# Performance work log

Hardware: AMD Instinct MI355X
Metric: run time of the kernel (lower is better)

Reference implementation:

```python
import jax, jax.numpy as jnp
import numpy as np

EPS = 1e-12  # torch F.normalize default eps
NUM_HEADS = 8


def _l2norm(t):
    # normalize along last (spatial) axis, matching F.normalize(dim=-1)
    n = jnp.linalg.norm(t, axis=-1, keepdims=True)
    return t / jnp.maximum(n, EPS)


def setup_inputs() -> dict:
    key = jax.random.key(0)
    ks = jax.random.split(key, 5)
    b, dim, qc, h, w = 16, 384, 192, 64, 64
    x = jax.random.normal(ks[0], (b, dim, h, w), dtype=jnp.float32)
    query = jax.random.normal(ks[1], (b, qc, h, w), dtype=jnp.float32)
    w_kv = jax.random.normal(ks[2], (2 * dim, dim), dtype=jnp.float32) * 0.05
    w_q = jax.random.normal(ks[3], (dim, qc), dtype=jnp.float32) * 0.05
    w_proj = jax.random.normal(ks[4], (dim, dim), dtype=jnp.float32) * 0.05
    temperature = jnp.ones((NUM_HEADS, 1, 1), dtype=jnp.float32)
    return {"x": x, "query": query, "w_kv": w_kv, "w_q": w_q,
            "w_proj": w_proj, "temperature": temperature}


def reference(x, query, w_kv, w_q, w_proj, temperature):
    b, c, h, w = x.shape
    hd = NUM_HEADS
    dc = c // hd  # per-head channel dim
    # 1x1 convs == channel GEMMs
    kv = jnp.einsum('oc,bchw->bohw', w_kv, x)          # [b, 2c, h, w]
    k, v = jnp.split(kv, 2, axis=1)                     # each [b, c, h, w]
    q = jnp.einsum('oc,bchw->bohw', w_q, query)         # [b, c, h, w]
    # split heads, flatten spatial: b (head c) h w -> b head c (h w)
    def heads(t):
        return t.reshape(b, hd, dc, h * w)
    q, k, v = heads(q), heads(k), heads(v)
    q = _l2norm(q)
    k = _l2norm(k)
    # channel-wise attention: [b, head, dc, dc]
    attn = jnp.einsum('bhcn,bhdn->bhcd', q, k) * temperature
    attn = jax.nn.softmax(attn, axis=-1)
    out = jnp.einsum('bhcd,bhdn->bhcn', attn, v)        # [b, head, dc, hw]
    out = out.reshape(b, c, h, w)
    out = jnp.einsum('oc,bchw->bohw', w_proj, out)
    return out
```

## Files before the change

kernel.cpp:

```cpp
#include <hip/hip_runtime.h>
#include <hip/hip_bf16.h>

typedef float f4 __attribute__((ext_vector_type(4)));
typedef short s8 __attribute__((ext_vector_type(8)));
typedef short s4 __attribute__((ext_vector_type(4)));

__device__ __forceinline__ short f2bf(float f) {
  union { float f; unsigned u; } v; v.f = f;
  unsigned r = v.u + 0x7fffu + ((v.u >> 16) & 1u);
  return (short)(r >> 16);
}
__device__ __forceinline__ void gl16(const short* g, short* l) {
  __builtin_amdgcn_global_load_lds(
      (const __attribute__((address_space(1))) unsigned*)g,
      (__attribute__((address_space(3))) unsigned*)l, 16, 0, 0);
}

template<int NKT, bool SUMSQ, bool OUTF32, bool SWZ>
__global__ __launch_bounds__(256)
void gemm4(const short* __restrict__ A_, long Asb, int lda,
           const short* __restrict__ B_, long Bsb, int ldb,
           void* __restrict__ O_, long Osb, int ldo,
           float* __restrict__ ss, int nbm, int nbn) {
  __shared__ __align__(16) short As[2][8192];
  __shared__ __align__(16) short Bs[2][8192];
  int f = blockIdx.x;
  if (SWZ) { const int cpx = gridDim.x >> 3; f = (f & 7) * cpx + (f >> 3); }
  const int m0 = (f % nbm) * 128;
  const int t2 = f / nbm;
  const int n0 = (t2 % nbn) * 128;
  const int bz = t2 / nbn;
  const short* Ag = A_ + (long)bz * Asb;
  const short* Bg = B_ + (long)bz * Bsb;

  const int tid = threadIdx.x, lane = tid & 63, wid = tid >> 6;
  const int l15 = lane & 15, lhi = lane >> 4;
  const int wm = (wid >> 1) * 64, wn = (wid & 1) * 64;
  const int srow = tid >> 3;
  const int skc = ((tid & 7) ^ (srow & 7)) * 8;

  f4 acc[4][4];
#pragma unroll
  for (int i = 0; i < 4; ++i)
#pragma unroll
    for (int j = 0; j < 4; ++j) acc[i][j] = (f4){0.f, 0.f, 0.f, 0.f};

#pragma unroll
  for (int it = 0; it < 4; ++it) {
    const int r = it * 32 + srow;
    gl16(Ag + (long)(m0 + r) * lda + skc, &As[0][(it * 256 + tid) * 8]);
    gl16(Bg + (long)(n0 + r) * ldb + skc, &Bs[0][(it * 256 + tid) * 8]);
  }
  if (NKT > 1) {
#pragma unroll
    for (int it = 0; it < 4; ++it) {
      const int r = it * 32 + srow;
      gl16(Ag + (long)(m0 + r) * lda + 64 + skc, &As[1][(it * 256 + tid) * 8]);
      gl16(Bg + (long)(n0 + r) * ldb + 64 + skc, &Bs[1][(it * 256 + tid) * 8]);
    }
  }

#pragma unroll
  for (int kt = 0; kt < NKT; ++kt) {
    const int cur = kt & 1;
    if (kt + 1 < NKT) asm volatile("s_waitcnt vmcnt(8)" ::: "memory");
    else              asm volatile("s_waitcnt vmcnt(0)" ::: "memory");
    __builtin_amdgcn_s_barrier();
    __builtin_amdgcn_sched_barrier(0);
#pragma unroll
    for (int kk = 0; kk < 2; ++kk) {
      const int cb = ((lhi + kk * 4) ^ (l15 & 7)) * 8;
      s8 af[4], bf[4];
#pragma unroll
      for (int i = 0; i < 4; ++i) {
        af[i] = *(const s8*)(&As[cur][(wm + i * 16 + l15) * 64 + cb]);
        bf[i] = *(const s8*)(&Bs[cur][(wn + i * 16 + l15) * 64 + cb]);
      }
#pragma unroll
      for (int mi = 0; mi < 4; ++mi)
#pragma unroll
        for (int ni = 0; ni < 4; ++ni)
          acc[mi][ni] = __builtin_amdgcn_mfma_f32_16x16x32_bf16(
              af[mi], bf[ni], acc[mi][ni], 0, 0, 0);
    }
    asm volatile("s_waitcnt lgkmcnt(0)" ::: "memory");
    __builtin_amdgcn_s_barrier();
    if (kt + 2 < NKT) {
      const int k2 = (kt + 2) * 64;
#pragma unroll
      for (int it = 0; it < 4; ++it) {
        const int r = it * 32 + srow;
        gl16(Ag + (long)(m0 + r) * lda + k2 + skc,
             &As[cur][(it * 256 + tid) * 8]);
        gl16(Bg + (long)(n0 + r) * ldb + k2 + skc,
             &Bs[cur][(it * 256 + tid) * 8]);
      }
    }
  }

#pragma unroll
  for (int mi = 0; mi < 4; ++mi)
#pragma unroll
    for (int r = 0; r < 4; ++r) {
      const int grow = m0 + wm + mi * 16 + lhi * 4 + r;
      if (SUMSQ) {
        float t = 0.f;
#pragma unroll
        for (int ni = 0; ni < 4; ++ni) { float v = acc[mi][ni][r]; t += v * v; }
        t += __shfl_xor(t, 1);
        t += __shfl_xor(t, 2);
        t += __shfl_xor(t, 4);
        t += __shfl_xor(t, 8);
        if (l15 == 0) atomicAdd(&ss[bz * 384 + grow], t);
      }
#pragma unroll
      for (int ni = 0; ni < 4; ++ni) {
        const int col = n0 + wn + ni * 16 + l15;
        const float v = acc[mi][ni][r];
        if (OUTF32)
          ((float*)O_)[(long)bz * Osb + (long)grow * ldo + col] = v;
        else
          ((short*)O_)[(long)bz * Osb + (long)grow * ldo + col] = f2bf(v);
      }
    }
}

__global__ __launch_bounds__(256)
void trans_k(const float* __restrict__ src, short* __restrict__ dst, int C) {
  __shared__ float Ls[64][65];
  const int tid = threadIdx.x;
  const int c0 = blockIdx.x * 64, s0 = blockIdx.y * 64;
  const long bb = (long)blockIdx.z * C * 4096;
  const int rr = tid >> 4;
  const int cq = (tid & 15) * 4;
#pragma unroll
  for (int it = 0; it < 4; ++it) {
    const int r = it * 16 + rr;
    f4 v = *(const f4*)(src + bb + (long)(c0 + r) * 4096 + s0 + cq);
    Ls[r][cq + 0] = v.x; Ls[r][cq + 1] = v.y;
    Ls[r][cq + 2] = v.z; Ls[r][cq + 3] = v.w;
  }
  __syncthreads();
  const long ob = (long)blockIdx.z * 4096 * C;
#pragma unroll
  for (int it = 0; it < 4; ++it) {
    const int sr = it * 16 + rr;
    s4 o;
#pragma unroll
    for (int j = 0; j < 4; ++j) o[j] = f2bf(Ls[cq + j][sr]);
    *(s4*)(&dst[ob + (long)(s0 + sr) * C + c0 + cq]) = o;
  }
}

__global__ __launch_bounds__(256)
void attn_k(const short* __restrict__ Kb, const short* __restrict__ Qb,
            float* __restrict__ Spart) {
  const int b = blockIdx.x, h = blockIdx.y, z = blockIdx.z;
  const int tid = threadIdx.x;
  const int lane = tid & 63, wid = tid >> 6;
  const int l15 = lane & 15, lhi = lane >> 4;
  const long base = ((long)b * 384 + h * 48) * 4096;

  f4 acc[3][3];
#pragma unroll
  for (int i = 0; i < 3; ++i)
#pragma unroll
    for (int j = 0; j < 3; ++j) acc[i][j] = (f4){0.f, 0.f, 0.f, 0.f};

  const int sb = z * 1024 + wid * 256;
  for (int st = 0; st < 8; ++st) {
    const int s0 = sb + st * 32 + lhi * 8;
    s8 qa[3], ka[3];
#pragma unroll
    for (int i = 0; i < 3; ++i) {
      qa[i] = *(const s8*)(Qb + base + (long)(i * 16 + l15) * 4096 + s0);
      ka[i] = *(const s8*)(Kb + base + (long)(i * 16 + l15) * 4096 + s0);
    }
#pragma unroll
    for (int mi = 0; mi < 3; ++mi)
#pragma unroll
      for (int ni = 0; ni < 3; ++ni)
        acc[mi][ni] = __builtin_amdgcn_mfma_f32_16x16x32_bf16(
            qa[mi], ka[ni], acc[mi][ni], 0, 0, 0);
  }
  __shared__ float Sl[2304];
  for (int i = tid; i < 2304; i += 256) Sl[i] = 0.f;
  __syncthreads();
#pragma unroll
  for (int mi = 0; mi < 3; ++mi)
#pragma unroll
    for (int ni = 0; ni < 3; ++ni)
#pragma unroll
      for (int r = 0; r < 4; ++r) {
        int c = mi * 16 + lhi * 4 + r;
        int d = ni * 16 + l15;
        atomicAdd(&Sl[c * 48 + d], acc[mi][ni][r]);
      }
  __syncthreads();
  float* op = Spart + (((long)z * 16 + b) * 8 + h) * 2304;
  for (int i = tid; i < 2304; i += 256) op[i] = Sl[i];
}

__global__ __launch_bounds__(256)
void softmax_k(const float* __restrict__ Spart, const float* __restrict__ ssq,
               const float* __restrict__ ssk, const float* __restrict__ temp,
               short* __restrict__ PT) {
  const int b = blockIdx.x, h = blockIdx.y, tid = threadIdx.x;
  __shared__ float L[2304];
  __shared__ float rq[48], rk[48], mrow[48], irow[48];
  if (tid < 48) {
    rq[tid] = 1.f / fmaxf(sqrtf(ssq[b * 384 + h * 48 + tid]), 1e-12f);
    rk[tid] = 1.f / fmaxf(sqrtf(ssk[b * 384 + h * 48 + tid]), 1e-12f);
  }
  __syncthreads();
  const float tp = temp[h];
  for (int i = tid; i < 2304; i += 256) {
    float v = 0.f;
#pragma unroll
    for (int z = 0; z < 4; ++z)
      v += Spart[(((long)z * 16 + b) * 8 + h) * 2304 + i];
    const int c = i / 48, d = i % 48;
    L[i] = v * rq[c] * rk[d] * tp;
  }
  __syncthreads();
  if (tid < 48) {
    float m = -1e30f;
    for (int d = 0; d < 48; ++d) m = fmaxf(m, L[tid * 48 + d]);
    float s = 0.f;
    for (int d = 0; d < 48; ++d) s += __expf(L[tid * 48 + d] - m);
    mrow[tid] = m;
    irow[tid] = 1.f / s;
  }
  __syncthreads();
  for (int i = tid; i < 18432; i += 256) {
    const int d = i / 384, c = i % 384;
    const int ch = c - h * 48;
    float p = 0.f;
    if (ch >= 0 && ch < 48) p = __expf(L[ch * 48 + d] - mrow[ch]) * irow[ch];
    PT[((long)b * 384 + h * 48 + d) * 384 + c] = f2bf(p);
  }
}

__global__ void wprep_k(const float* __restrict__ wkv, const float* __restrict__ wq,
                        const float* __restrict__ wp, short* __restrict__ wkb,
                        short* __restrict__ wvT, short* __restrict__ wqb,
                        short* __restrict__ wpb, float* __restrict__ ssqk) {
  const int i = blockIdx.x * 256 + threadIdx.x;
  if (i < 12288) ssqk[i] = 0.f;
  if (i < 147456) {
    wkb[i] = f2bf(wkv[i]);
  } else if (i < 294912) {
    const int t = i - 147456;
    wvT[t] = f2bf(wkv[(384 + (t % 384)) * 384 + t / 384]);
  } else if (i < 368640) {
    wqb[i - 294912] = f2bf(wq[i - 294912]);
  } else {
    wpb[i - 368640] = f2bf(wp[i - 368640]);
  }
}

extern "C" void kernel_launch(void* const* d_in, const int* in_sizes, int n_in,
                              void* d_out, int out_size, void* d_ws, size_t ws_size,
                              hipStream_t stream) {
  const float* x = (const float*)d_in[0];
  const float* query = (const float*)d_in[1];
  const float* w_kv = (const float*)d_in[2];
  const float* w_q = (const float*)d_in[3];
  const float* w_proj = (const float*)d_in[4];
  const float* temp = (const float*)d_in[5];

  char* w = (char*)d_ws;
  short* xT   = (short*)(w + 0);
  short* qT   = (short*)(w + 50331648);
  short* Kb   = (short*)(w + 75497472);
  short* Qb   = (short*)(w + 125829120);
  float* Spart= (float*)(w + 176160768);
  short* PTb  = (short*)(w + 195035136);
  short* Yb   = (short*)(w + 199753728);
  short* Nbb  = (short*)(w + 204472320);
  float* ssq  = (float*)(w + 209190912);
  float* ssk  = (float*)(w + 209215488);
  short* wkb  = (short*)(w + 209240064);
  short* wvT  = (short*)(w + 209534976);
  short* wqb  = (short*)(w + 209829888);
  short* wpb  = (short*)(w + 209977344);
  float* out  = (float*)d_out;

  wprep_k<<<2016, 256, 0, stream>>>(w_kv, w_q, w_proj, wkb, wvT, wqb, wpb, ssq);
  trans_k<<<dim3(6, 64, 16), 256, 0, stream>>>(x, xT, 384);
  trans_k<<<dim3(3, 64, 16), 256, 0, stream>>>(query, qT, 192);
  gemm4<3, true, false, true><<<1536, 256, 0, stream>>>(
      wqb, 0, 192, qT, 786432, 192, Qb, 1572864, 4096, ssq, 3, 32);
  gemm4<6, true, false, true><<<1536, 256, 0, stream>>>(
      wkb, 0, 384, xT, 1572864, 384, Kb, 1572864, 4096, ssk, 3, 32);
  attn_k<<<dim3(16, 8, 4), 256, 0, stream>>>(Kb, Qb, Spart);
  softmax_k<<<dim3(16, 8), 256, 0, stream>>>(Spart, ssq, ssk, temp, PTb);
  gemm4<6, false, false, false><<<144, 256, 0, stream>>>(
      wpb, 0, 384, PTb, 147456, 384, Yb, 147456, 384, nullptr, 3, 3);
  gemm4<6, false, false, false><<<144, 256, 0, stream>>>(
      Yb, 147456, 384, wvT, 0, 384, Nbb, 147456, 384, nullptr, 3, 3);
  gemm4<6, false, true, true><<<1536, 256, 0, stream>>>(
      Nbb, 147456, 384, xT, 1572864, 384, out, 1572864, 4096, nullptr, 3, 32);
}
```

Before: 229.8 us.

## Fuse Q/K projections with channel-attention scores into one kernel

```diff
diff --git a/kernel.cpp b/kernel.cpp
--- a/kernel.cpp
+++ b/kernel.cpp
@@ -16,12 +16,171 @@
       (__attribute__((address_space(3))) unsigned*)l, 16, 0, 0);
 }
 
-template<int NKT, bool SUMSQ, bool OUTF32, bool SWZ>
+__global__ __launch_bounds__(256)
+void kqa_k(const short* __restrict__ xT, const short* __restrict__ qT,
+           const short* __restrict__ wkb, const short* __restrict__ wqb,
+           float* __restrict__ Spart, float* __restrict__ ssq,
+           float* __restrict__ ssk) {
+  __shared__ __align__(16) short Bq[64 * 192];
+  __shared__ __align__(16) short Bx[64 * 384];
+  __shared__ __align__(16) short Qt[192 * 64];
+  __shared__ __align__(16) short Kt[192 * 64];
+  const int f = blockIdx.x;
+  const int sl = f & 63, hg = (f >> 6) & 1, b = f >> 7;
+  const int s0 = sl * 64;
+  const int tid = threadIdx.x, lane = tid & 63, w = tid >> 6;
+  const int l15 = lane & 15, lhi = lane >> 4;
+  const short* qTb = qT + ((long)b * 4096 + s0) * 192;
+  const short* xTb = xT + ((long)b * 4096 + s0) * 384;
+
+#pragma unroll
+  for (int i = 0; i < 6; ++i) {
+    const int q = i * 256 + tid, row = q / 24, c = q % 24;
+    gl16(qTb + row * 192 + ((c ^ (row & 7)) * 8), &Bq[q * 8]);
+  }
+#pragma unroll
+  for (int i = 0; i < 12; ++i) {
+    const int q = i * 256 + tid, row = q / 48, c = q % 48;
+    gl16(xTb + row * 384 + ((c ^ (row & 7)) * 8), &Bx[q * 8]);
+  }
+  asm volatile("s_waitcnt vmcnt(12)" ::: "memory");
+  __builtin_amdgcn_s_barrier();
+  __builtin_amdgcn_sched_barrier(0);
+
+  {
+    f4 acc[3][4];
+#pragma unroll
+    for (int i = 0; i < 3; ++i)
+#pragma unroll
+      for (int j = 0; j < 4; ++j) acc[i][j] = (f4){0.f, 0.f, 0.f, 0.f};
+#pragma unroll 2
+    for (int kk = 0; kk < 192; kk += 32) {
+      s8 af[3], bf[4];
+#pragma unroll
+      for (int mi = 0; mi < 3; ++mi)
+        af[mi] = *(const s8*)(wqb +
+            (long)(hg * 192 + w * 48 + mi * 16 + l15) * 192 + kk + lhi * 8);
+#pragma unroll
+      for (int ni = 0; ni < 4; ++ni) {
+        const int s_ = ni * 16 + l15;
+        bf[ni] = *(const s8*)(&Bq[s_ * 192 + ((((kk >> 3) + lhi) ^ (s_ & 7)) << 3)]);
+      }
+#pragma unroll
+      for (int mi = 0; mi < 3; ++mi)
+#pragma unroll
+        for (int ni = 0; ni < 4; ++ni)
+          acc[mi][ni] = __builtin_amdgcn_mfma_f32_16x16x32_bf16(
+              af[mi], bf[ni], acc[mi][ni], 0, 0, 0);
+    }
+#pragma unroll
+    for (int mi = 0; mi < 3; ++mi)
+#pragma unroll
+      for (int r = 0; r < 4; ++r) {
+        const int row = w * 48 + mi * 16 + lhi * 4 + r;
+        float t = 0.f;
+#pragma unroll
+        for (int ni = 0; ni < 4; ++ni) {
+          const int col = ni * 16 + l15;
+          const float v = acc[mi][ni][r];
+          Qt[row * 64 + (((col >> 3) ^ (row & 7)) << 3) + (col & 7)] = f2bf(v);
+          t += v * v;
+        }
+        t += __shfl_xor(t, 1); t += __shfl_xor(t, 2);
+        t += __shfl_xor(t, 4); t += __shfl_xor(t, 8);
+        if (l15 == 0) atomicAdd(&ssq[b * 384 + hg * 192 + row], t);
+      }
+  }
+
+  asm volatile("s_waitcnt vmcnt(0)" ::: "memory");
+  __builtin_amdgcn_s_barrier();
+  __builtin_amdgcn_sched_barrier(0);
+
+  {
+    f4 acc[3][4];
+#pragma unroll
+    for (int i = 0; i < 3; ++i)
+#pragma unroll
+      for (int j = 0; j < 4; ++j) acc[i][j] = (f4){0.f, 0.f, 0.f, 0.f};
+#pragma unroll 2
+    for (int kk = 0; kk < 384; kk += 32) {
+      s8 af[3], bf[4];
+#pragma unroll
+      for (int mi = 0; mi < 3; ++mi)
+        af[mi] = *(const s8*)(wkb +
+            (long)(hg * 192 + w * 48 + mi * 16 + l15) * 384 + kk + lhi * 8);
+#pragma unroll
+      for (int ni = 0; ni < 4; ++ni) {
+        const int s_ = ni * 16 + l15;
+        bf[ni] = *(const s8*)(&Bx[s_ * 384 + ((((kk >> 3) + lhi) ^ (s_ & 7)) << 3)]);
+      }
+#pragma unroll
+      for (int mi = 0; mi < 3; ++mi)
+#pragma unroll
+        for (int ni = 0; ni < 4; ++ni)
+          acc[mi][ni] = __builtin_amdgcn_mfma_f32_16x16x32_bf16(
+              af[mi], bf[ni], acc[mi][ni], 0, 0, 0);
+    }
+#pragma unroll
+    for (int mi = 0; mi < 3; ++mi)
+#pragma unroll
+      for (int r = 0; r < 4; ++r) {
+        const int row = w * 48 + mi * 16 + lhi * 4 + r;
+        float t = 0.f;
+#pragma unroll
+        for (int ni = 0; ni < 4; ++ni) {
+          const int col = ni * 16 + l15;
+          const float v = acc[mi][ni][r];
+          Kt[row * 64 + (((col >> 3) ^ (row & 7)) << 3) + (col & 7)] = f2bf(v);
+          t += v * v;
+        }
+        t += __shfl_xor(t, 1); t += __shfl_xor(t, 2);
+        t += __shfl_xor(t, 4); t += __shfl_xor(t, 8);
+        if (l15 == 0) atomicAdd(&ssk[b * 384 + hg * 192 + row], t);
+      }
+  }
+
+  {
+    f4 acc[3][3];
+#pragma unroll
+    for (int i = 0; i < 3; ++i)
+#pragma unroll
+      for (int j = 0; j < 3; ++j) acc[i][j] = (f4){0.f, 0.f, 0.f, 0.f};
+    const int hl = w * 48;
+#pragma unroll
+    for (int kk = 0; kk < 64; kk += 32) {
+      s8 qa[3], ka[3];
+#pragma unroll
+      for (int i = 0; i < 3; ++i) {
+        const int rr = hl + i * 16 + l15;
+        const int cb = (((kk >> 3) + lhi) ^ (rr & 7)) << 3;
+        qa[i] = *(const s8*)(&Qt[rr * 64 + cb]);
+        ka[i] = *(const s8*)(&Kt[rr * 64 + cb]);
+      }
+#pragma unroll
+      for (int mi = 0; mi < 3; ++mi)
+#pragma unroll
+        for (int ni = 0; ni < 3; ++ni)
+          acc[mi][ni] = __builtin_amdgcn_mfma_f32_16x16x32_bf16(
+              qa[mi], ka[ni], acc[mi][ni], 0, 0, 0);
+    }
+    float* Sp = Spart + (((long)(sl & 7) * 16 + b) * 8 + (hg * 4 + w)) * 2304;
+#pragma unroll
+    for (int mi = 0; mi < 3; ++mi)
+#pragma unroll
+      for (int ni = 0; ni < 3; ++ni)
+#pragma unroll
+        for (int r = 0; r < 4; ++r)
+          atomicAdd(&Sp[(mi * 16 + lhi * 4 + r) * 48 + ni * 16 + l15],
+                    acc[mi][ni][r]);
+  }
+}
+
+template<int NKT, bool OUTF32, bool SWZ>
 __global__ __launch_bounds__(256)
 void gemm4(const short* __restrict__ A_, long Asb, int lda,
            const short* __restrict__ B_, long Bsb, int ldb,
            void* __restrict__ O_, long Osb, int ldo,
-           float* __restrict__ ss, int nbm, int nbn) {
+           int nbm, int nbn) {
   __shared__ __align__(16) short As[2][8192];
   __shared__ __align__(16) short Bs[2][8192];
   int f = blockIdx.x;
@@ -103,16 +262,6 @@
 #pragma unroll
     for (int r = 0; r < 4; ++r) {
       const int grow = m0 + wm + mi * 16 + lhi * 4 + r;
-      if (SUMSQ) {
-        float t = 0.f;
-#pragma unroll
-        for (int ni = 0; ni < 4; ++ni) { float v = acc[mi][ni][r]; t += v * v; }
-        t += __shfl_xor(t, 1);
-        t += __shfl_xor(t, 2);
-        t += __shfl_xor(t, 4);
-        t += __shfl_xor(t, 8);
-        if (l15 == 0) atomicAdd(&ss[bz * 384 + grow], t);
-      }
 #pragma unroll
       for (int ni = 0; ni < 4; ++ni) {
         const int col = n0 + wn + ni * 16 + l15;
@@ -150,55 +299,6 @@
     for (int j = 0; j < 4; ++j) o[j] = f2bf(Ls[cq + j][sr]);
     *(s4*)(&dst[ob + (long)(s0 + sr) * C + c0 + cq]) = o;
   }
-}
-
-__global__ __launch_bounds__(256)
-void attn_k(const short* __restrict__ Kb, const short* __restrict__ Qb,
-            float* __restrict__ Spart) {
-  const int b = blockIdx.x, h = blockIdx.y, z = blockIdx.z;
-  const int tid = threadIdx.x;
-  const int lane = tid & 63, wid = tid >> 6;
-  const int l15 = lane & 15, lhi = lane >> 4;
-  const long base = ((long)b * 384 + h * 48) * 4096;
-
-  f4 acc[3][3];
-#pragma unroll
-  for (int i = 0; i < 3; ++i)
-#pragma unroll
-    for (int j = 0; j < 3; ++j) acc[i][j] = (f4){0.f, 0.f, 0.f, 0.f};
-
-  const int sb = z * 1024 + wid * 256;
-  for (int st = 0; st < 8; ++st) {
-    const int s0 = sb + st * 32 + lhi * 8;
-    s8 qa[3], ka[3];
-#pragma unroll
-    for (int i = 0; i < 3; ++i) {
-      qa[i] = *(const s8*)(Qb + base + (long)(i * 16 + l15) * 4096 + s0);
-      ka[i] = *(const s8*)(Kb + base + (long)(i * 16 + l15) * 4096 + s0);
-    }
-#pragma unroll
-    for (int mi = 0; mi < 3; ++mi)
-#pragma unroll
-      for (int ni = 0; ni < 3; ++ni)
-        acc[mi][ni] = __builtin_amdgcn_mfma_f32_16x16x32_bf16(
-            qa[mi], ka[ni], acc[mi][ni], 0, 0, 0);
-  }
-  __shared__ float Sl[2304];
-  for (int i = tid; i < 2304; i += 256) Sl[i] = 0.f;
-  __syncthreads();
-#pragma unroll
-  for (int mi = 0; mi < 3; ++mi)
-#pragma unroll
-    for (int ni = 0; ni < 3; ++ni)
-#pragma unroll
-      for (int r = 0; r < 4; ++r) {
-        int c = mi * 16 + lhi * 4 + r;
-        int d = ni * 16 + l15;
-        atomicAdd(&Sl[c * 48 + d], acc[mi][ni][r]);
-      }
-  __syncthreads();
-  float* op = Spart + (((long)z * 16 + b) * 8 + h) * 2304;
-  for (int i = tid; i < 2304; i += 256) op[i] = Sl[i];
 }
 
 __global__ __launch_bounds__(256)
@@ -217,7 +317,7 @@
   for (int i = tid; i < 2304; i += 256) {
     float v = 0.f;
 #pragma unroll
-    for (int z = 0; z < 4; ++z)
+    for (int z = 0; z < 8; ++z)
       v += Spart[(((long)z * 16 + b) * 8 + h) * 2304 + i];
     const int c = i / 48, d = i % 48;
     L[i] = v * rq[c] * rk[d] * tp;
@@ -244,9 +344,11 @@
 __global__ void wprep_k(const float* __restrict__ wkv, const float* __restrict__ wq,
                         const float* __restrict__ wp, short* __restrict__ wkb,
                         short* __restrict__ wvT, short* __restrict__ wqb,
-                        short* __restrict__ wpb, float* __restrict__ ssqk) {
+                        short* __restrict__ wpb, float* __restrict__ ssqk,
+                        float* __restrict__ Spart) {
   const int i = blockIdx.x * 256 + threadIdx.x;
   if (i < 12288) ssqk[i] = 0.f;
+  for (int j = i; j < 2359296; j += 516096) Spart[j] = 0.f;
   if (i < 147456) {
     wkb[i] = f2bf(wkv[i]);
   } else if (i < 294912) {
@@ -272,33 +374,28 @@
   char* w = (char*)d_ws;
   short* xT   = (short*)(w + 0);
   short* qT   = (short*)(w + 50331648);
-  short* Kb   = (short*)(w + 75497472);
-  short* Qb   = (short*)(w + 125829120);
-  float* Spart= (float*)(w + 176160768);
-  short* PTb  = (short*)(w + 195035136);
-  short* Yb   = (short*)(w + 199753728);
-  short* Nbb  = (short*)(w + 204472320);
-  float* ssq  = (float*)(w + 209190912);
-  float* ssk  = (float*)(w + 209215488);
-  short* wkb  = (short*)(w + 209240064);
-  short* wvT  = (short*)(w + 209534976);
-  short* wqb  = (short*)(w + 209829888);
-  short* wpb  = (short*)(w + 209977344);
+  float* Spart= (float*)(w + 75497472);
+  short* PTb  = (short*)(w + 84934656);
+  short* Yb   = (short*)(w + 89653248);
+  short* Nbb  = (short*)(w + 94371840);
+  float* ssq  = (float*)(w + 99090432);
+  float* ssk  = (float*)(w + 99115008);
+  short* wkb  = (short*)(w + 99139584);
+  short* wvT  = (short*)(w + 99434496);
+  short* wqb  = (short*)(w + 99729408);
+  short* wpb  = (short*)(w + 99876864);
   float* out  = (float*)d_out;
 
-  wprep_k<<<2016, 256, 0, stream>>>(w_kv, w_q, w_proj, wkb, wvT, wqb, wpb, ssq);
+  wprep_k<<<2016, 256, 0, stream>>>(w_kv, w_q, w_proj, wkb, wvT, wqb, wpb,
+                                    ssq, Spart);
   trans_k<<<dim3(6, 64, 16), 256, 0, stream>>>(x, xT, 384);
   trans_k<<<dim3(3, 64, 16), 256, 0, stream>>>(query, qT, 192);
-  gemm4<3, true, false, true><<<1536, 256, 0, stream>>>(
-      wqb, 0, 192, qT, 786432, 192, Qb, 1572864, 4096, ssq, 3, 32);
-  gemm4<6, true, false, true><<<1536, 256, 0, stream>>>(
-      wkb, 0, 384, xT, 1572864, 384, Kb, 1572864, 4096, ssk, 3, 32);
-  attn_k<<<dim3(16, 8, 4), 256, 0, stream>>>(Kb, Qb, Spart);
+  kqa_k<<<2048, 256, 0, stream>>>(xT, qT, wkb, wqb, Spart, ssq, ssk);
   softmax_k<<<dim3(16, 8), 256, 0, stream>>>(Spart, ssq, ssk, temp, PTb);
-  gemm4<6, false, false, false><<<144, 256, 0, stream>>>(
-      wpb, 0, 384, PTb, 147456, 384, Yb, 147456, 384, nullptr, 3, 3);
-  gemm4<6, false, false, false><<<144, 256, 0, stream>>>(
-      Yb, 147456, 384, wvT, 0, 384, Nbb, 147456, 384, nullptr, 3, 3);
-  gemm4<6, false, true, true><<<1536, 256, 0, stream>>>(
-      Nbb, 147456, 384, xT, 1572864, 384, out, 1572864, 4096, nullptr, 3, 32);
-}
+  gemm4<6, false, false><<<144, 256, 0, stream>>>(
+      wpb, 0, 384, PTb, 147456, 384, Yb, 147456, 384, 3, 3);
+  gemm4<6, false, false><<<144, 256, 0, stream>>>(
+      Yb, 147456, 384, wvT, 0, 384, Nbb, 147456, 384, 3, 3);
+  gemm4<6, true, true><<<1536, 256, 0, stream>>>(
+      Nbb, 147456, 384, xT, 1572864, 384, out, 1572864, 4096, 3, 32);
+}
```

Measured after the change: 282.8 us. 1.23x slower.

## Merge transpose and K/Q GEMM launches, fuse softmax with w_proj GEMM

Applied to the files above, without the earlier changes.

```diff
diff --git a/kernel.cpp b/kernel.cpp
--- a/kernel.cpp
+++ b/kernel.cpp
@@ -16,12 +16,114 @@
       (__attribute__((address_space(3))) unsigned*)l, 16, 0, 0);
 }
 
-template<int NKT, bool SUMSQ, bool OUTF32, bool SWZ>
+__global__ __launch_bounds__(256)
+void kq_k(const short* __restrict__ wkb, const short* __restrict__ wqb,
+          const short* __restrict__ xT, const short* __restrict__ qT,
+          short* __restrict__ Kb, short* __restrict__ Qb,
+          float* __restrict__ ssk, float* __restrict__ ssq) {
+  __shared__ __align__(16) short As[2][8192];
+  __shared__ __align__(16) short Bs[2][8192];
+  int f = blockIdx.x;
+  f = (f & 7) * 384 + (f >> 3);
+  const bool isQ = f >= 1536;
+  const int g = isQ ? f - 1536 : f;
+  const int m0 = (g % 3) * 128;
+  const int t2 = g / 3;
+  const int n0 = (t2 & 31) * 128;
+  const int bz = t2 >> 5;
+  const int lda = isQ ? 192 : 384;
+  const int nkt = isQ ? 3 : 6;
+  const short* Ag = isQ ? wqb : wkb;
+  const short* Bg = (isQ ? qT + (long)bz * 786432 : xT + (long)bz * 1572864);
+  short* Og = (isQ ? Qb : Kb) + (long)bz * 1572864;
+  float* ss = (isQ ? ssq : ssk) + bz * 384;
+
+  const int tid = threadIdx.x, lane = tid & 63, wid = tid >> 6;
+  const int l15 = lane & 15, lhi = lane >> 4;
+  const int wm = (wid >> 1) * 64, wn = (wid & 1) * 64;
+  const int srow = tid >> 3;
+  const int skc = ((tid & 7) ^ (srow & 7)) * 8;
+
+  f4 acc[4][4];
+#pragma unroll
+  for (int i = 0; i < 4; ++i)
+#pragma unroll
+    for (int j = 0; j < 4; ++j) acc[i][j] = (f4){0.f, 0.f, 0.f, 0.f};
+
+#pragma unroll
+  for (int it = 0; it < 4; ++it) {
+    const int r = it * 32 + srow;
+    gl16(Ag + (long)(m0 + r) * lda + skc, &As[0][(it * 256 + tid) * 8]);
+    gl16(Bg + (long)(n0 + r) * lda + skc, &Bs[0][(it * 256 + tid) * 8]);
+  }
+#pragma unroll
+  for (int it = 0; it < 4; ++it) {
+    const int r = it * 32 + srow;
+    gl16(Ag + (long)(m0 + r) * lda + 64 + skc, &As[1][(it * 256 + tid) * 8]);
+    gl16(Bg + (long)(n0 + r) * lda + 64 + skc, &Bs[1][(it * 256 + tid) * 8]);
+  }
+
+#pragma unroll 1
+  for (int kt = 0; kt < nkt; ++kt) {
+    const int cur = kt & 1;
+    if (kt + 1 < nkt) asm volatile("s_waitcnt vmcnt(8)" ::: "memory");
+    else              asm volatile("s_waitcnt vmcnt(0)" ::: "memory");
+    __builtin_amdgcn_s_barrier();
+    __builtin_amdgcn_sched_barrier(0);
+#pragma unroll
+    for (int kk = 0; kk < 2; ++kk) {
+      const int cb = ((lhi + kk * 4) ^ (l15 & 7)) * 8;
+      s8 af[4], bf[4];
+#pragma unroll
+      for (int i = 0; i < 4; ++i) {
+        af[i] = *(const s8*)(&As[cur][(wm + i * 16 + l15) * 64 + cb]);
+        bf[i] = *(const s8*)(&Bs[cur][(wn + i * 16 + l15) * 64 + cb]);
+      }
+#pragma unroll
+      for (int mi = 0; mi < 4; ++mi)
+#pragma unroll
+        for (int ni = 0; ni < 4; ++ni)
+          acc[mi][ni] = __builtin_amdgcn_mfma_f32_16x16x32_bf16(
+              af[mi], bf[ni], acc[mi][ni], 0, 0, 0);
+    }
+    asm volatile("s_waitcnt lgkmcnt(0)" ::: "memory");
+    __builtin_amdgcn_s_barrier();
+    if (kt + 2 < nkt) {
+      const int k2 = (kt + 2) * 64;
+#pragma unroll
+      for (int it = 0; it < 4; ++it) {
+        const int r = it * 32 + srow;
+        gl16(Ag + (long)(m0 + r) * lda + k2 + skc,
+             &As[cur][(it * 256 + tid) * 8]);
+        gl16(Bg + (long)(n0 + r) * lda + k2 + skc,
+             &Bs[cur][(it * 256 + tid) * 8]);
+      }
+    }
+  }
+
+#pragma unroll
+  for (int mi = 0; mi < 4; ++mi)
+#pragma unroll
+    for (int r = 0; r < 4; ++r) {
+      const int grow = m0 + wm + mi * 16 + lhi * 4 + r;
+      float t = 0.f;
+#pragma unroll
+      for (int ni = 0; ni < 4; ++ni) { float v = acc[mi][ni][r]; t += v * v; }
+      t += __shfl_xor(t, 1); t += __shfl_xor(t, 2);
+      t += __shfl_xor(t, 4); t += __shfl_xor(t, 8);
+      if (l15 == 0) atomicAdd(&ss[grow], t);
+#pragma unroll
+      for (int ni = 0; ni < 4; ++ni)
+        Og[(long)grow * 4096 + n0 + wn + ni * 16 + l15] = f2bf(acc[mi][ni][r]);
+    }
+}
+
+template<int NKT, bool OUTF32, bool SWZ>
 __global__ __launch_bounds__(256)
 void gemm4(const short* __restrict__ A_, long Asb, int lda,
            const short* __restrict__ B_, long Bsb, int ldb,
            void* __restrict__ O_, long Osb, int ldo,
-           float* __restrict__ ss, int nbm, int nbn) {
+           int nbm, int nbn) {
   __shared__ __align__(16) short As[2][8192];
   __shared__ __align__(16) short Bs[2][8192];
   int f = blockIdx.x;
@@ -103,16 +205,6 @@
 #pragma unroll
     for (int r = 0; r < 4; ++r) {
       const int grow = m0 + wm + mi * 16 + lhi * 4 + r;
-      if (SUMSQ) {
-        float t = 0.f;
-#pragma unroll
-        for (int ni = 0; ni < 4; ++ni) { float v = acc[mi][ni][r]; t += v * v; }
-        t += __shfl_xor(t, 1);
-        t += __shfl_xor(t, 2);
-        t += __shfl_xor(t, 4);
-        t += __shfl_xor(t, 8);
-        if (l15 == 0) atomicAdd(&ss[bz * 384 + grow], t);
-      }
 #pragma unroll
       for (int ni = 0; ni < 4; ++ni) {
         const int col = n0 + wn + ni * 16 + l15;
@@ -126,29 +218,33 @@
 }
 
 __global__ __launch_bounds__(256)
-void trans_k(const float* __restrict__ src, short* __restrict__ dst, int C) {
+void prep_k(const float* __restrict__ x, const float* __restrict__ q,
+            short* __restrict__ xT, short* __restrict__ qT) {
   __shared__ float Ls[64][65];
+  const int role = blockIdx.x;
+  const bool isQ = role >= 6;
+  const int C = isQ ? 192 : 384;
+  const int c0 = (isQ ? role - 6 : role) * 64;
+  const int s0 = blockIdx.y * 64;
+  const float* src = (isQ ? q : x) + (long)blockIdx.z * C * 4096;
+  short* dst = (isQ ? qT : xT) + (long)blockIdx.z * 4096 * C;
   const int tid = threadIdx.x;
-  const int c0 = blockIdx.x * 64, s0 = blockIdx.y * 64;
-  const long bb = (long)blockIdx.z * C * 4096;
-  const int rr = tid >> 4;
-  const int cq = (tid & 15) * 4;
+  const int rr = tid >> 4, cq = (tid & 15) * 4;
 #pragma unroll
   for (int it = 0; it < 4; ++it) {
     const int r = it * 16 + rr;
-    f4 v = *(const f4*)(src + bb + (long)(c0 + r) * 4096 + s0 + cq);
+    f4 v = *(const f4*)(src + (long)(c0 + r) * 4096 + s0 + cq);
     Ls[r][cq + 0] = v.x; Ls[r][cq + 1] = v.y;
     Ls[r][cq + 2] = v.z; Ls[r][cq + 3] = v.w;
   }
   __syncthreads();
-  const long ob = (long)blockIdx.z * 4096 * C;
 #pragma unroll
   for (int it = 0; it < 4; ++it) {
     const int sr = it * 16 + rr;
     s4 o;
 #pragma unroll
     for (int j = 0; j < 4; ++j) o[j] = f2bf(Ls[cq + j][sr]);
-    *(s4*)(&dst[ob + (long)(s0 + sr) * C + c0 + cq]) = o;
+    *(s4*)(&dst[(long)(s0 + sr) * C + c0 + cq]) = o;
   }
 }
 
@@ -202,12 +298,13 @@
 }
 
 __global__ __launch_bounds__(256)
-void softmax_k(const float* __restrict__ Spart, const float* __restrict__ ssq,
-               const float* __restrict__ ssk, const float* __restrict__ temp,
-               short* __restrict__ PT) {
+void smY_k(const float* __restrict__ Spart, const float* __restrict__ ssq,
+           const float* __restrict__ ssk, const float* __restrict__ temp,
+           const short* __restrict__ wpb, short* __restrict__ Yb) {
   const int b = blockIdx.x, h = blockIdx.y, tid = threadIdx.x;
   __shared__ float L[2304];
   __shared__ float rq[48], rk[48], mrow[48], irow[48];
+  __shared__ __align__(16) short PTl[48 * 72];
   if (tid < 48) {
     rq[tid] = 1.f / fmaxf(sqrtf(ssq[b * 384 + h * 48 + tid]), 1e-12f);
     rk[tid] = 1.f / fmaxf(sqrtf(ssk[b * 384 + h * 48 + tid]), 1e-12f);
@@ -232,13 +329,47 @@
     irow[tid] = 1.f / s;
   }
   __syncthreads();
-  for (int i = tid; i < 18432; i += 256) {
-    const int d = i / 384, c = i % 384;
-    const int ch = c - h * 48;
+  for (int i = tid; i < 48 * 72; i += 256) {
+    const int d = i / 72, c = i % 72;
     float p = 0.f;
-    if (ch >= 0 && ch < 48) p = __expf(L[ch * 48 + d] - mrow[ch]) * irow[ch];
-    PT[((long)b * 384 + h * 48 + d) * 384 + c] = f2bf(p);
-  }
+    if (c < 48) p = __expf(L[c * 48 + d] - mrow[c]) * irow[c];
+    PTl[i] = f2bf(p);
+  }
+  __syncthreads();
+  const int lane = tid & 63, w = tid >> 6;
+  const int l15 = lane & 15, lhi = lane >> 4;
+  f4 acc[6][3];
+#pragma unroll
+  for (int i = 0; i < 6; ++i)
+#pragma unroll
+    for (int j = 0; j < 3; ++j) acc[i][j] = (f4){0.f, 0.f, 0.f, 0.f};
+#pragma unroll
+  for (int kk = 0; kk < 2; ++kk) {
+    s8 bf[3];
+#pragma unroll
+    for (int ni = 0; ni < 3; ++ni)
+      bf[ni] = *(const s8*)(&PTl[(ni * 16 + l15) * 72 + kk * 32 + lhi * 8]);
+#pragma unroll
+    for (int mi = 0; mi < 6; ++mi) {
+      const int row = w * 96 + mi * 16 + l15;
+      s8 af = *(const s8*)(wpb + (long)row * 384 + h * 48 + kk * 32 + lhi * 8);
+#pragma unroll
+      for (int ni = 0; ni < 3; ++ni)
+        acc[mi][ni] = __builtin_amdgcn_mfma_f32_16x16x32_bf16(
+            af, bf[ni], acc[mi][ni], 0, 0, 0);
+    }
+  }
+#pragma unroll
+  for (int mi = 0; mi < 6; ++mi)
+#pragma unroll
+    for (int r = 0; r < 4; ++r) {
+      const int row = w * 96 + mi * 16 + lhi * 4 + r;
+#pragma unroll
+      for (int ni = 0; ni < 3; ++ni) {
+        const int d = ni * 16 + l15;
+        Yb[((long)b * 384 + row) * 384 + h * 48 + d] = f2bf(acc[mi][ni][r]);
+      }
+    }
 }
 
 __global__ void wprep_k(const float* __restrict__ wkv, const float* __restrict__ wq,
@@ -275,30 +406,23 @@
   short* Kb   = (short*)(w + 75497472);
   short* Qb   = (short*)(w + 125829120);
   float* Spart= (float*)(w + 176160768);
-  short* PTb  = (short*)(w + 195035136);
-  short* Yb   = (short*)(w + 199753728);
-  short* Nbb  = (short*)(w + 204472320);
-  float* ssq  = (float*)(w + 209190912);
-  float* ssk  = (float*)(w + 209215488);
-  short* wkb  = (short*)(w + 209240064);
-  short* wvT  = (short*)(w + 209534976);
-  short* wqb  = (short*)(w + 209829888);
-  short* wpb  = (short*)(w + 209977344);
+  short* Yb   = (short*)(w + 180879360);
+  short* Nbb  = (short*)(w + 185597952);
+  float* ssq  = (float*)(w + 190316544);
+  float* ssk  = (float*)(w + 190341120);
+  short* wkb  = (short*)(w + 190365696);
+  short* wvT  = (short*)(w + 190660608);
+  short* wqb  = (short*)(w + 190955520);
+  short* wpb  = (short*)(w + 191102976);
   float* out  = (float*)d_out;
 
   wprep_k<<<2016, 256, 0, stream>>>(w_kv, w_q, w_proj, wkb, wvT, wqb, wpb, ssq);
-  trans_k<<<dim3(6, 64, 16), 256, 0, stream>>>(x, xT, 384);
-  trans_k<<<dim3(3, 64, 16), 256, 0, stream>>>(query, qT, 192);
-  gemm4<3, true, false, true><<<1536, 256, 0, stream>>>(
-      wqb, 0, 192, qT, 786432, 192, Qb, 1572864, 4096, ssq, 3, 32);
-  gemm4<6, true, false, true><<<1536, 256, 0, stream>>>(
-      wkb, 0, 384, xT, 1572864, 384, Kb, 1572864, 4096, ssk, 3, 32);
+  prep_k<<<dim3(9, 64, 16), 256, 0, stream>>>(x, query, xT, qT);
+  kq_k<<<3072, 256, 0, stream>>>(wkb, wqb, xT, qT, Kb, Qb, ssk, ssq);
   attn_k<<<dim3(16, 8, 4), 256, 0, stream>>>(Kb, Qb, Spart);
-  softmax_k<<<dim3(16, 8), 256, 0, stream>>>(Spart, ssq, ssk, temp, PTb);
-  gemm4<6, false, false, false><<<144, 256, 0, stream>>>(
-      wpb, 0, 384, PTb, 147456, 384, Yb, 147456, 384, nullptr, 3, 3);
-  gemm4<6, false, false, false><<<144, 256, 0, stream>>>(
-      Yb, 147456, 384, wvT, 0, 384, Nbb, 147456, 384, nullptr, 3, 3);
-  gemm4<6, false, true, true><<<1536, 256, 0, stream>>>(
-      Nbb, 147456, 384, xT, 1572864, 384, out, 1572864, 4096, nullptr, 3, 32);
-}
+  smY_k<<<dim3(16, 8), 256, 0, stream>>>(Spart, ssq, ssk, temp, wpb, Yb);
+  gemm4<6, false, false><<<144, 256, 0, stream>>>(
+      Yb, 147456, 384, wvT, 0, 384, Nbb, 147456, 384, 3, 3);
+  gemm4<6, true, true><<<1536, 256, 0, stream>>>(
+      Nbb, 147456, 384, xT, 1572864, 384, out, 1572864, 4096, 3, 32);
+}
```

Measured after the change: 215.7 us. 1.07x faster.
